# Performance work log

Measured on AMD Instinct MI355X. Metric: run time of the kernel, lower is better.

## Reference

```python
import jax, jax.numpy as jnp
import numpy as np
from jax import lax

B, S, H, SS, DS = 512, 200, 128, 2, 2  # batch, seq_len, hidden, static_size, dynamic_size

def _xavier(k, shape):
    fan_in, fan_out = shape[-1], shape[0]
    lim = float(np.sqrt(6.0 / (fan_in + fan_out)))
    return jax.random.uniform(k, shape, jnp.float32, -lim, lim)

def setup_inputs() -> dict:
    key = jax.random.key(0)
    ks = jax.random.split(key, 20)
    return {
        "static":  jax.random.uniform(ks[0], (B, SS, S), jnp.float32),
        "dynamic": jax.random.uniform(ks[1], (B, DS, S), jnp.float32),
        # Encoder: 1x1 Conv1d weights stored as [H, C] (kernel dim squeezed)
        "sW": _xavier(ks[2], (H, SS)),  "sb": jnp.zeros((H,), jnp.float32),
        "dW": _xavier(ks[3], (H, DS)),  "db": jnp.zeros((H,), jnp.float32),
        # Decoder learned initial output / hidden
        "x0": _xavier(ks[4], (1, SS)),  "h0": _xavier(ks[5], (1, H)),
        # Decoder input embedding Linear(SS -> H)
        "Wemb": _xavier(ks[6], (H, SS)), "bemb": jnp.zeros((H,), jnp.float32),
        # GRU (1 layer): torch layout [3H, H] gates ordered (r, z, n)
        "Wih": _xavier(ks[7], (3 * H, H)), "Whh": _xavier(ks[8], (3 * H, H)),
        "bih": jnp.zeros((3 * H,), jnp.float32), "bhh": jnp.zeros((3 * H,), jnp.float32),
        # Attention: v [H], W [H, 3H]
        "Wa": _xavier(ks[9], (H, 3 * H)), "va": _xavier(ks[10], (1, H))[0],
        # Decoder pointer head: v [H], W [H, 2H]
        "Wd": _xavier(ks[11], (H, 2 * H)), "vd": _xavier(ks[12], (1, H))[0],
    }

def _decode(static, dynamic, sW, sb, dW, db, x0, h0, Wemb, bemb,
            Wih, Whh, bih, bhh, Wa, va, Wd, vd):
    # Encoder: 1x1 convs == per-node linear maps  -> [B, H, S]
    static_enc  = jnp.einsum('hc,bcs->bhs', sW, static)  + sb[None, :, None]
    dynamic_enc = jnp.einsum('hc,bcs->bhs', dW, dynamic) + db[None, :, None]

    keys = jax.random.split(jax.random.key(42), S)  # one sample key per decode step
    static_sg = lax.stop_gradient(static)           # mirrors static.data gather in torch

    def step(carry, key):
        last_out, h = carry                              # [B,SS], [B,H]
        emb = last_out @ Wemb.T + bemb                   # [B,H]
        # GRU cell (torch gate order r, z, n)
        gi = emb @ Wih.T + bih                           # [B,3H]
        gh = h @ Whh.T + bhh
        r = jax.nn.sigmoid(gi[:, :H] + gh[:, :H])
        z = jax.nn.sigmoid(gi[:, H:2 * H] + gh[:, H:2 * H])
        n = jnp.tanh(gi[:, 2 * H:] + r * gh[:, 2 * H:])
        h_new = (1.0 - z) * n + z * h                    # [B,H]
        # Additive attention over nodes (vectorized over batch)
        hid = jnp.broadcast_to(h_new[:, :, None], (B, H, S))
        energy = jnp.concatenate([static_enc, dynamic_enc, hid], axis=1)   # [B,3H,S]
        attn = jax.nn.softmax(
            jnp.einsum('h,bhs->bs', va, jnp.tanh(jnp.einsum('hk,bks->bhs', Wa, energy))),
            axis=1)                                      # [B,S]
        context = jnp.einsum('bs,bhs->bh', attn, static_enc)               # [B,H]
        ctx = jnp.concatenate(
            [static_enc, jnp.broadcast_to(context[:, :, None], (B, H, S))], axis=1)  # [B,2H,S]
        logits = jnp.einsum('h,bhs->bs', vd,
                            jnp.tanh(jnp.einsum('hk,bks->bhs', Wd, ctx)))  # [B,S]
        # mask is all ones (mask_fn=None) -> log(mask)=0
        probs = jax.nn.softmax(logits, axis=1)
        idx = jax.random.categorical(key, logits, axis=1)                  # [B] int
        next_out = jnp.take_along_axis(static_sg, idx[:, None, None], axis=2)[:, :, 0]  # [B,SS]
        chosen_p = jnp.take_along_axis(probs, idx[:, None], axis=1)[:, 0]  # [B]
        return (next_out, h_new), (idx, chosen_p)

    init = (jnp.broadcast_to(x0, (B, SS)), jnp.broadcast_to(h0, (B, H)))
    _, (idx_seq, prob_seq) = lax.scan(step, init, keys)
    return idx_seq.T, prob_seq.T                          # [B,S] each

def reference(static, dynamic, sW, sb, dW, db, x0, h0, Wemb, bemb,
              Wih, Whh, bih, bhh, Wa, va, Wd, vd):
    return _decode(static, dynamic, sW, sb, dW, db, x0, h0, Wemb, bemb,
                   Wih, Whh, bih, bhh, Wa, va, Wd, vd)
```

## Files before the change

kernel.cpp:

```cpp
#include <hip/hip_runtime.h>
#include <stdint.h>
#include <math.h>

#define NB 512
#define NS 200
#define NH 128
#define NH3 384
#define NWAVE 8

#define IDX4(h) ((h) + (((h) >> 6) << 2))
#define IDX2(h) ((h) + (((h) >> 6) << 3))

__device__ __forceinline__ float xla_tanhf(float x) {
  float cx = fminf(fmaxf(x, -9.0f), 9.0f);
  float x2 = __fmul_rn(cx, cx);
  float p = -2.76076847742355e-16f;
  p = __fadd_rn(__fmul_rn(x2, p), 2.00018790482477e-13f);
  p = __fadd_rn(__fmul_rn(x2, p), -8.60467152213735e-11f);
  p = __fadd_rn(__fmul_rn(x2, p), 5.12229709037114e-08f);
  p = __fadd_rn(__fmul_rn(x2, p), 1.48572235717979e-05f);
  p = __fadd_rn(__fmul_rn(x2, p), 6.37261928875436e-04f);
  p = __fadd_rn(__fmul_rn(x2, p), 4.89352455891786e-03f);
  p = __fmul_rn(cx, p);
  float q = 1.19825839466702e-06f;
  q = __fadd_rn(__fmul_rn(x2, q), 1.18534705686654e-04f);
  q = __fadd_rn(__fmul_rn(x2, q), 2.26843463243900e-03f);
  q = __fadd_rn(__fmul_rn(x2, q), 4.89352518554385e-03f);
  float r = __fdiv_rn(p, q);
  return (fabsf(x) < 0.0004f) ? x : r;
}

__device__ __forceinline__ float xla_sigmoidf(float x) {
  return __fadd_rn(0.5f, __fmul_rn(0.5f, xla_tanhf(__fmul_rn(0.5f, x))));
}

__device__ __forceinline__ uint32_t rotl32(uint32_t v, int r) {
  return (v << r) | (v >> (32 - r));
}
__device__ __forceinline__ void threefry2x32(uint32_t k0, uint32_t k1,
                                             uint32_t x0, uint32_t x1,
                                             uint32_t& o0, uint32_t& o1) {
  uint32_t k2 = k0 ^ k1 ^ 0x1BD11BDAu;
  x0 += k0; x1 += k1;
  #define TFR(r) { x0 += x1; x1 = rotl32(x1, r); x1 ^= x0; }
  TFR(13) TFR(15) TFR(26) TFR(6)
  x0 += k1; x1 += k2 + 1u;
  TFR(17) TFR(29) TFR(16) TFR(24)
  x0 += k2; x1 += k0 + 2u;
  TFR(13) TFR(15) TFR(26) TFR(6)
  x0 += k0; x1 += k1 + 3u;
  TFR(17) TFR(29) TFR(16) TFR(24)
  x0 += k1; x1 += k2 + 4u;
  TFR(13) TFR(15) TFR(26) TFR(6)
  x0 += k2; x1 += k0 + 5u;
  #undef TFR
  o0 = x0; o1 = x1;
}

__device__ __forceinline__ float bits_to_gumbel(uint32_t bits) {
  const float kTiny = 1.1754943508222875e-38f;
  float f = __fsub_rn(__uint_as_float((bits >> 9) | 0x3F800000u), 1.0f);
  float u = __fadd_rn(__fmul_rn(f, __fsub_rn(1.0f, kTiny)), kTiny);
  u = fmaxf(kTiny, u);
  return -logf(-logf(u));
}

__global__ __launch_bounds__(512, 4) void k_decode(
    const float* __restrict__ stat, const float* __restrict__ dyn,
    const float* __restrict__ sW,   const float* __restrict__ sb,
    const float* __restrict__ dW,   const float* __restrict__ db,
    const float* __restrict__ x0,   const float* __restrict__ h0,
    const float* __restrict__ Wemb, const float* __restrict__ bemb,
    const float* __restrict__ Wih,  const float* __restrict__ Whh,
    const float* __restrict__ bih,  const float* __restrict__ bhh,
    const float* __restrict__ Wa,   const float* __restrict__ va,
    const float* __restrict__ Wd,   const float* __restrict__ vd,
    float* __restrict__ out) {

  __shared__ __align__(16) float st0L[NS], st1L[NS], dy0L[NS], dy1L[NS];
  __shared__ float4 AF4p[132];
  __shared__ float4 DF4p[132];
  __shared__ float4 CW4[NH];
  __shared__ float2 HtVaP[136];
  __shared__ float  AcL[NH];
  __shared__ float WembL[2*NH], bembL[NH];
  __shared__ float bihL[NH3], bhhL[NH3];
  __shared__ __align__(16) float embL[NH], hL[NH];
  __shared__ float giL[NH3], ghL[NH3];
  __shared__ float ex2L[NS], gumL[NS];
  __shared__ uint32_t keysL[2*NS];
  __shared__ float xpL[2];
  __shared__ float SvL[2];
  __shared__ float part[NWAVE][8];
  __shared__ int   partI[NWAVE];

  const int t = threadIdx.x;
  const int b = blockIdx.x;
  const int w = t >> 6;
  const int s = t >> 1;
  const int h0i = (t & 1) * 64;
  const int b4 = h0i + ((h0i >> 6) << 2);
  const int b2 = h0i + ((h0i >> 6) << 3);
  const bool activeS = (t < 2*NS);

  if (t < NS) {
    st0L[t] = stat[(size_t)b*2*NS + t];
    st1L[t] = stat[(size_t)b*2*NS + NS + t];
    dy0L[t] = dyn[(size_t)b*2*NS + t];
    dy1L[t] = dyn[(size_t)b*2*NS + NS + t];
    uint32_t q0, q1;
    threefry2x32(0u, 42u, 0u, (uint32_t)t, q0, q1);
    keysL[2*t] = q0; keysL[2*t + 1] = q1;
  }
  if (t < NH) {
    int h = t;
    const float* war = Wa + (size_t)h * NH3;
    float as0 = 0.f, as1 = 0.f, ad0 = 0.f, ad1 = 0.f, ac = 0.f;
    for (int k = 0; k < NH; ++k) {
      as0 = fmaf(war[k],     sW[k*2+0], as0);
      as1 = fmaf(war[k],     sW[k*2+1], as1);
      ad0 = fmaf(war[NH+k],  dW[k*2+0], ad0);
      ad1 = fmaf(war[NH+k],  dW[k*2+1], ad1);
      ac  = fmaf(war[k],     sb[k],     ac);
    }
    for (int k = 0; k < NH; ++k) ac = fmaf(war[NH+k], db[k], ac);
    AF4p[IDX4(h)] = make_float4(2.f*as0, 2.f*as1, 2.f*ad0, 2.f*ad1);
    HtVaP[IDX2(h)] = make_float2(va[h], 0.f);
    AcL[h] = ac;

    const float* wdr = Wd + (size_t)h * 256;
    float ds0 = 0.f, ds1 = 0.f, dc = 0.f, c0 = 0.f, c1 = 0.f, cb = 0.f;
    for (int k = 0; k < NH; ++k) {
      ds0 = fmaf(wdr[k],    sW[k*2+0], ds0);
      ds1 = fmaf(wdr[k],    sW[k*2+1], ds1);
      dc  = fmaf(wdr[k],    sb[k],     dc);
      c0  = fmaf(wdr[NH+k], sW[k*2+0], c0);
      c1  = fmaf(wdr[NH+k], sW[k*2+1], c1);
      cb  = fmaf(wdr[NH+k], sb[k],     cb);
    }
    DF4p[IDX4(h)] = make_float4(2.f*ds0, 2.f*ds1, vd[h], 0.f);
    CW4[h] = make_float4(2.f*c0, 2.f*c1, 2.f*cb, 2.f*dc);

    bembL[h] = bemb[h];
    WembL[2*h]   = Wemb[2*h];
    WembL[2*h+1] = Wemb[2*h+1];
    hL[h] = h0[h];
  }
  for (int i = t; i < NH3; i += 512) { bihL[i] = bih[i]; bhhL[i] = bhh[i]; }
  if (t == 0) {
    xpL[0] = x0[0]; xpL[1] = x0[1];
    float sva = 0.f, svd = 0.f;
    for (int h = 0; h < NH; ++h) { sva = __fadd_rn(sva, va[h]); svd = __fadd_rn(svd, vd[h]); }
    SvL[0] = sva; SvL[1] = svd;
  }
  __syncthreads();

  float s0r = 0.f, s1r = 0.f, d0r = 0.f, d1r = 0.f;
  if (activeS) { s0r = st0L[s]; s1r = st1L[s]; d0r = dy0L[s]; d1r = dy1L[s]; }
  const float svaR = SvL[0], svdR = SvL[1];

  for (int step = 0; step < NS; ++step) {
    if (t < NH) {
      float e = fmaf(xpL[1], WembL[t*2+1], __fmul_rn(xpL[0], WembL[t*2+0]));
      embL[t] = __fadd_rn(e, bembL[t]);
    } else if (t < NH + NS) {
      int si = t - NH;
      uint32_t k0 = keysL[2*step], k1 = keysL[2*step + 1];
      uint32_t q0, q1;
      threefry2x32(k0, k1, 0u, (uint32_t)(b*NS + si), q0, q1);
      gumL[si] = bits_to_gumbel(q0 ^ q1);
    }
    __syncthreads();

    if (t < 256) {
      const float4* wp0 = (const float4*)(Wih + (size_t)t * NH);
      const float4* wp1 = (const float4*)(Whh + (size_t)(NH + t) * NH);
      const float4* e4 = (const float4*)embL;
      const float4* h4 = (const float4*)hL;
      float a0 = 0.f, a1 = 0.f;
      #pragma unroll 8
      for (int k4 = 0; k4 < 32; ++k4) {
        float4 c0 = wp0[k4], c1 = wp1[k4];
        float4 ev = e4[k4],  hv = h4[k4];
        a0 = fmaf(c0.x, ev.x, a0); a0 = fmaf(c0.y, ev.y, a0);
        a0 = fmaf(c0.z, ev.z, a0); a0 = fmaf(c0.w, ev.w, a0);
        a1 = fmaf(c1.x, hv.x, a1); a1 = fmaf(c1.y, hv.y, a1);
        a1 = fmaf(c1.z, hv.z, a1); a1 = fmaf(c1.w, hv.w, a1);
      }
      giL[t]      = __fadd_rn(a0, bihL[t]);
      ghL[NH + t] = __fadd_rn(a1, bhhL[NH + t]);
    } else {
      const bool isWih = (t < NH3);
      const float4* wp = isWih
          ? (const float4*)(Wih + (size_t)t * NH)
          : (const float4*)(Whh + (size_t)(t - NH3) * NH);
      const float4* op = isWih ? (const float4*)embL : (const float4*)hL;
      float a0 = 0.f;
      #pragma unroll 8
      for (int k4 = 0; k4 < 32; ++k4) {
        float4 c = wp[k4], v = op[k4];
        a0 = fmaf(c.x, v.x, a0); a0 = fmaf(c.y, v.y, a0);
        a0 = fmaf(c.z, v.z, a0); a0 = fmaf(c.w, v.w, a0);
      }
      if (isWih) giL[t]       = __fadd_rn(a0, bihL[t]);
      else       ghL[t - NH3] = __fadd_rn(a0, bhhL[t - NH3]);
    }
    __syncthreads();

    if (t < NH) {
      float r = xla_sigmoidf(__fadd_rn(giL[t],      ghL[t]));
      float z = xla_sigmoidf(__fadd_rn(giL[t+NH],   ghL[t+NH]));
      float n = xla_tanhf(__fadd_rn(giL[t+2*NH], __fmul_rn(r, ghL[t+2*NH])));
      float hv = hL[t];
      hL[t] = __fadd_rn(__fmul_rn(__fsub_rn(1.0f, z), n), __fmul_rn(z, hv));
    }
    __syncthreads();

    if (t < NH) {
      const float4* war = (const float4*)(Wa + (size_t)t*NH3 + 2*NH);
      const float4* hn4 = (const float4*)hL;
      float acc = 0.f;
      #pragma unroll 8
      for (int k4 = 0; k4 < 32; ++k4) {
        float4 a = war[k4], hv = hn4[k4];
        acc = fmaf(a.x, hv.x, acc); acc = fmaf(a.y, hv.y, acc);
        acc = fmaf(a.z, hv.z, acc); acc = fmaf(a.w, hv.w, acc);
      }
      HtVaP[IDX2(t)].y = __fmul_rn(2.0f, __fadd_rn(acc, AcL[t]));
    }
    __syncthreads();

    float accE = 0.f;
    if (activeS) {
      #pragma unroll 4
      for (int j = 0; j < 64; ++j) {
        float4 af = AF4p[b4 + j];
        float2 hv = HtVaP[b2 + j];
        float e2 = fmaf(af.x, s0r, hv.y);
        e2 = fmaf(af.y, s1r, e2);
        e2 = fmaf(af.z, d0r, e2);
        e2 = fmaf(af.w, d1r, e2);
        float r = __builtin_amdgcn_rcpf(__fadd_rn(__expf(e2), 1.0f));
        accE = fmaf(hv.x, r, accE);
      }
    }
    float accSum = __fadd_rn(accE, __shfl_xor(accE, 1));
    float sc = activeS ? fmaf(-2.0f, accSum, svaR) : 0.f;

    float exv = activeS ? __expf(sc) : 0.f;
    {
      float sm = exv;
      float c0 = __fmul_rn(exv, s0r);
      float c1 = __fmul_rn(exv, s1r);
      #pragma unroll
      for (int mm = 2; mm < 64; mm <<= 1) {
        sm = __fadd_rn(sm, __shfl_xor(sm, mm));
        c0 = __fadd_rn(c0, __shfl_xor(c0, mm));
        c1 = __fadd_rn(c1, __shfl_xor(c1, mm));
      }
      if ((t & 63) == 0) { part[w][0] = sm; part[w][1] = c0; part[w][2] = c1; }
    }
    __syncthreads();

    if (t < NH) {
      float sume = part[0][0], r0 = part[0][1], r1 = part[0][2];
      #pragma unroll
      for (int ww = 1; ww < NWAVE; ++ww) {
        sume = __fadd_rn(sume, part[ww][0]);
        r0   = __fadd_rn(r0,   part[ww][1]);
        r1   = __fadd_rn(r1,   part[ww][2]);
      }
      r0 = __fdiv_rn(r0, sume); r1 = __fdiv_rn(r1, sume);
      float4 cw = CW4[t];
      float ct2 = fmaf(r0, cw.x, fmaf(r1, cw.y, cw.z));
      DF4p[IDX4(t)].w = __fadd_rn(cw.w, ct2);
    }
    __syncthreads();

    float accD = 0.f;
    if (activeS) {
      #pragma unroll 4
      for (int j = 0; j < 64; ++j) {
        float4 df = DF4p[b4 + j];
        float d2 = fmaf(df.x, s0r, df.w);
        d2 = fmaf(df.y, s1r, d2);
        float r = __builtin_amdgcn_rcpf(__fadd_rn(__expf(d2), 1.0f));
        accD = fmaf(df.z, r, accD);
      }
    }
    float accDS = __fadd_rn(accD, __shfl_xor(accD, 1));
    float sc2 = activeS ? fmaf(-2.0f, accDS, svdR) : 0.f;

    float e2 = activeS ? __expf(sc2) : 0.f;
    if (activeS && (t & 1) == 0) ex2L[s] = e2;
    {
      float gv = -INFINITY;
      int gidx = 1 << 20;
      if (activeS) {
        gv = __fadd_rn(gumL[s], sc2);
        gidx = s;
      }
      float sm = e2;
      #pragma unroll
      for (int mm = 2; mm < 64; mm <<= 1) {
        sm = __fadd_rn(sm, __shfl_xor(sm, mm));
        float ov = __shfl_xor(gv, mm); int oi = __shfl_xor(gidx, mm);
        if (ov > gv || (ov == gv && oi < gidx)) { gv = ov; gidx = oi; }
      }
      if ((t & 63) == 0) { part[w][3] = sm; part[w][4] = gv; partI[w] = gidx; }
    }
    __syncthreads();

    if (t == 0) {
      float bv = part[0][4]; int bi = partI[0];
      float sume2 = part[0][3];
      #pragma unroll
      for (int ww = 1; ww < NWAVE; ++ww) {
        float vv = part[ww][4]; int ii = partI[ww];
        if (vv > bv || (vv == bv && ii < bi)) { bv = vv; bi = ii; }
        sume2 = __fadd_rn(sume2, part[ww][3]);
      }
      out[(size_t)b*NS + step] = (float)bi;
      out[(size_t)NB*NS + (size_t)b*NS + step] = __fdiv_rn(ex2L[bi], sume2);
      xpL[0] = st0L[bi]; xpL[1] = st1L[bi];
    }
    __syncthreads();
  }
}

extern "C" void kernel_launch(void* const* d_in, const int* in_sizes, int n_in,
                              void* d_out, int out_size, void* d_ws, size_t ws_size,
                              hipStream_t stream) {
  (void)in_sizes; (void)n_in; (void)out_size; (void)d_ws; (void)ws_size;
  const float* stat = (const float*)d_in[0];
  const float* dyn  = (const float*)d_in[1];
  const float* sW   = (const float*)d_in[2];
  const float* sb   = (const float*)d_in[3];
  const float* dW   = (const float*)d_in[4];
  const float* db   = (const float*)d_in[5];
  const float* x0   = (const float*)d_in[6];
  const float* h0   = (const float*)d_in[7];
  const float* Wemb = (const float*)d_in[8];
  const float* bemb = (const float*)d_in[9];
  const float* Wih  = (const float*)d_in[10];
  const float* Whh  = (const float*)d_in[11];
  const float* bih  = (const float*)d_in[12];
  const float* bhh  = (const float*)d_in[13];
  const float* Wa   = (const float*)d_in[14];
  const float* va   = (const float*)d_in[15];
  const float* Wd   = (const float*)d_in[16];
  const float* vd   = (const float*)d_in[17];
  float* out = (float*)d_out;

  k_decode<<<NB, 512, 0, stream>>>(stat, dyn, sW, sb, dW, db, x0, h0,
                                   Wemb, bemb, Wih, Whh, bih, bhh,
                                   Wa, va, Wd, vd, out);
}
```

Before: 5.892 ms.

## Process two batch rows per block with 1024 threads sharing GRU weight loads

Each block now handles two batch elements (b and b+256) with 1024 threads. The GRU matvec loads each weight row once and applies it to both rows' embeddings and hidden states, which halves weight traffic per batch element. Per-row state is duplicated into A/B shared buffers, and the per-step reductions are split by half-block. The cost is half as many blocks (256 on the device), larger blocks with higher register and LDS pressure, and serial phases such as the attention matvec that still run on only 256 threads.

```diff
diff --git a/kernel.cpp b/kernel.cpp
--- a/kernel.cpp
+++ b/kernel.cpp
@@ -6,10 +6,11 @@
 #define NS 200
 #define NH 128
 #define NH3 384
-#define NWAVE 8
+#define NT 1024
+#define NWAVE 16
 
 #define IDX4(h) ((h) + (((h) >> 6) << 2))
-#define IDX2(h) ((h) + (((h) >> 6) << 3))
+#define IDX1(h) ((h) + (((h) >> 6) << 4))
 
 __device__ __forceinline__ float xla_tanhf(float x) {
   float cx = fminf(fmaxf(x, -9.0f), 9.0f);
@@ -65,7 +66,7 @@
   return -logf(-logf(u));
 }
 
-__global__ __launch_bounds__(512, 4) void k_decode(
+__global__ __launch_bounds__(NT, 4) void k_decode(
     const float* __restrict__ stat, const float* __restrict__ dyn,
     const float* __restrict__ sW,   const float* __restrict__ sb,
     const float* __restrict__ dW,   const float* __restrict__ db,
@@ -77,43 +78,55 @@
     const float* __restrict__ Wd,   const float* __restrict__ vd,
     float* __restrict__ out) {
 
-  __shared__ __align__(16) float st0L[NS], st1L[NS], dy0L[NS], dy1L[NS];
+  __shared__ __align__(16) float st0A[NS], st1A[NS], dy0A[NS], dy1A[NS];
+  __shared__ __align__(16) float st0B[NS], st1B[NS], dy0B[NS], dy1B[NS];
   __shared__ float4 AF4p[132];
-  __shared__ float4 DF4p[132];
+  __shared__ float4 DFSp[132];
   __shared__ float4 CW4[NH];
-  __shared__ float2 HtVaP[136];
+  __shared__ float  vaP[144];
+  __shared__ float  Ht2A[144], Ht2B[144];
+  __shared__ float  ct2A[144], ct2B[144];
   __shared__ float  AcL[NH];
   __shared__ float WembL[2*NH], bembL[NH];
   __shared__ float bihL[NH3], bhhL[NH3];
-  __shared__ __align__(16) float embL[NH], hL[NH];
-  __shared__ float giL[NH3], ghL[NH3];
-  __shared__ float ex2L[NS], gumL[NS];
+  __shared__ __align__(16) float embA[NH], embB[NH], hA[NH], hB[NH];
+  __shared__ float giA[NH3], ghA[NH3], giB[NH3], ghB[NH3];
+  __shared__ float ex2A[NS], ex2B[NS], gumA[NS], gumB[NS];
   __shared__ uint32_t keysL[2*NS];
-  __shared__ float xpL[2];
+  __shared__ float xpA[2], xpB[2];
   __shared__ float SvL[2];
   __shared__ float part[NWAVE][8];
   __shared__ int   partI[NWAVE];
 
   const int t = threadIdx.x;
-  const int b = blockIdx.x;
+  const int bA = blockIdx.x;
+  const int bB = blockIdx.x + 256;
   const int w = t >> 6;
-  const int s = t >> 1;
-  const int h0i = (t & 1) * 64;
+  const bool rB = (t >= 512);
+  const int tr = rB ? (t - 512) : t;
+  const int s = tr >> 1;
+  const int h0i = (tr & 1) * 64;
   const int b4 = h0i + ((h0i >> 6) << 2);
-  const int b2 = h0i + ((h0i >> 6) << 3);
-  const bool activeS = (t < 2*NS);
+  const int b1 = h0i + ((h0i >> 6) << 4);
+  const bool act = (tr < 2*NS);
 
   if (t < NS) {
-    st0L[t] = stat[(size_t)b*2*NS + t];
-    st1L[t] = stat[(size_t)b*2*NS + NS + t];
-    dy0L[t] = dyn[(size_t)b*2*NS + t];
-    dy1L[t] = dyn[(size_t)b*2*NS + NS + t];
+    st0A[t] = stat[(size_t)bA*2*NS + t];
+    st1A[t] = stat[(size_t)bA*2*NS + NS + t];
+    dy0A[t] = dyn[(size_t)bA*2*NS + t];
+    dy1A[t] = dyn[(size_t)bA*2*NS + NS + t];
     uint32_t q0, q1;
     threefry2x32(0u, 42u, 0u, (uint32_t)t, q0, q1);
     keysL[2*t] = q0; keysL[2*t + 1] = q1;
+  } else if (t >= 256 && t < 256 + NS) {
+    int si = t - 256;
+    st0B[si] = stat[(size_t)bB*2*NS + si];
+    st1B[si] = stat[(size_t)bB*2*NS + NS + si];
+    dy0B[si] = dyn[(size_t)bB*2*NS + si];
+    dy1B[si] = dyn[(size_t)bB*2*NS + NS + si];
   }
-  if (t < NH) {
-    int h = t;
+  if (t >= 512 && t < 512 + NH) {
+    int h = t - 512;
     const float* war = Wa + (size_t)h * NH3;
     float as0 = 0.f, as1 = 0.f, ad0 = 0.f, ad1 = 0.f, ac = 0.f;
     for (int k = 0; k < NH; ++k) {
@@ -125,7 +138,7 @@
     }
     for (int k = 0; k < NH; ++k) ac = fmaf(war[NH+k], db[k], ac);
     AF4p[IDX4(h)] = make_float4(2.f*as0, 2.f*as1, 2.f*ad0, 2.f*ad1);
-    HtVaP[IDX2(h)] = make_float2(va[h], 0.f);
+    vaP[IDX1(h)] = va[h];
     AcL[h] = ac;
 
     const float* wdr = Wd + (size_t)h * 256;
@@ -138,17 +151,19 @@
       c1  = fmaf(wdr[NH+k], sW[k*2+1], c1);
       cb  = fmaf(wdr[NH+k], sb[k],     cb);
     }
-    DF4p[IDX4(h)] = make_float4(2.f*ds0, 2.f*ds1, vd[h], 0.f);
+    DFSp[IDX4(h)] = make_float4(2.f*ds0, 2.f*ds1, vd[h], 0.f);
     CW4[h] = make_float4(2.f*c0, 2.f*c1, 2.f*cb, 2.f*dc);
 
     bembL[h] = bemb[h];
     WembL[2*h]   = Wemb[2*h];
     WembL[2*h+1] = Wemb[2*h+1];
-    hL[h] = h0[h];
+    hA[h] = h0[h];
+    hB[h] = h0[h];
   }
-  for (int i = t; i < NH3; i += 512) { bihL[i] = bih[i]; bhhL[i] = bhh[i]; }
+  for (int i = t; i < NH3; i += NT) { bihL[i] = bih[i]; bhhL[i] = bhh[i]; }
   if (t == 0) {
-    xpL[0] = x0[0]; xpL[1] = x0[1];
+    xpA[0] = x0[0]; xpA[1] = x0[1];
+    xpB[0] = x0[0]; xpB[1] = x0[1];
     float sva = 0.f, svd = 0.f;
     for (int h = 0; h < NH; ++h) { sva = __fadd_rn(sva, va[h]); svd = __fadd_rn(svd, vd[h]); }
     SvL[0] = sva; SvL[1] = svd;
@@ -156,69 +171,85 @@
   __syncthreads();
 
   float s0r = 0.f, s1r = 0.f, d0r = 0.f, d1r = 0.f;
-  if (activeS) { s0r = st0L[s]; s1r = st1L[s]; d0r = dy0L[s]; d1r = dy1L[s]; }
+  if (act) {
+    if (!rB) { s0r = st0A[s]; s1r = st1A[s]; d0r = dy0A[s]; d1r = dy1A[s]; }
+    else     { s0r = st0B[s]; s1r = st1B[s]; d0r = dy0B[s]; d1r = dy1B[s]; }
+  }
   const float svaR = SvL[0], svdR = SvL[1];
+  const float* HtX = rB ? Ht2B : Ht2A;
+  const float* ctX = rB ? ct2B : ct2A;
+  const float* gumX = rB ? gumB : gumA;
 
   for (int step = 0; step < NS; ++step) {
     if (t < NH) {
-      float e = fmaf(xpL[1], WembL[t*2+1], __fmul_rn(xpL[0], WembL[t*2+0]));
-      embL[t] = __fadd_rn(e, bembL[t]);
-    } else if (t < NH + NS) {
-      int si = t - NH;
+      float e = fmaf(xpA[1], WembL[t*2+1], __fmul_rn(xpA[0], WembL[t*2+0]));
+      embA[t] = __fadd_rn(e, bembL[t]);
+    } else if (t < 2*NH) {
+      int h = t - NH;
+      float e = fmaf(xpB[1], WembL[h*2+1], __fmul_rn(xpB[0], WembL[h*2+0]));
+      embB[h] = __fadd_rn(e, bembL[h]);
+    } else if (t < 2*NH + 2*NS) {
+      int gi = t - 2*NH;
       uint32_t k0 = keysL[2*step], k1 = keysL[2*step + 1];
       uint32_t q0, q1;
-      threefry2x32(k0, k1, 0u, (uint32_t)(b*NS + si), q0, q1);
-      gumL[si] = bits_to_gumbel(q0 ^ q1);
-    }
-    __syncthreads();
-
-    if (t < 256) {
-      const float4* wp0 = (const float4*)(Wih + (size_t)t * NH);
-      const float4* wp1 = (const float4*)(Whh + (size_t)(NH + t) * NH);
-      const float4* e4 = (const float4*)embL;
-      const float4* h4 = (const float4*)hL;
-      float a0 = 0.f, a1 = 0.f;
-      #pragma unroll 8
-      for (int k4 = 0; k4 < 32; ++k4) {
-        float4 c0 = wp0[k4], c1 = wp1[k4];
-        float4 ev = e4[k4],  hv = h4[k4];
-        a0 = fmaf(c0.x, ev.x, a0); a0 = fmaf(c0.y, ev.y, a0);
-        a0 = fmaf(c0.z, ev.z, a0); a0 = fmaf(c0.w, ev.w, a0);
-        a1 = fmaf(c1.x, hv.x, a1); a1 = fmaf(c1.y, hv.y, a1);
-        a1 = fmaf(c1.z, hv.z, a1); a1 = fmaf(c1.w, hv.w, a1);
-      }
-      giL[t]      = __fadd_rn(a0, bihL[t]);
-      ghL[NH + t] = __fadd_rn(a1, bhhL[NH + t]);
-    } else {
+      if (gi < NS) {
+        threefry2x32(k0, k1, 0u, (uint32_t)(bA*NS + gi), q0, q1);
+        gumA[gi] = bits_to_gumbel(q0 ^ q1);
+      } else {
+        int si = gi - NS;
+        threefry2x32(k0, k1, 0u, (uint32_t)(bB*NS + si), q0, q1);
+        gumB[si] = bits_to_gumbel(q0 ^ q1);
+      }
+    }
+    __syncthreads();
+
+    if (t < 2*NH3) {
       const bool isWih = (t < NH3);
       const float4* wp = isWih
           ? (const float4*)(Wih + (size_t)t * NH)
           : (const float4*)(Whh + (size_t)(t - NH3) * NH);
-      const float4* op = isWih ? (const float4*)embL : (const float4*)hL;
-      float a0 = 0.f;
+      const float4* opA = isWih ? (const float4*)embA : (const float4*)hA;
+      const float4* opB = isWih ? (const float4*)embB : (const float4*)hB;
+      float aA = 0.f, aB = 0.f;
       #pragma unroll 8
       for (int k4 = 0; k4 < 32; ++k4) {
-        float4 c = wp[k4], v = op[k4];
-        a0 = fmaf(c.x, v.x, a0); a0 = fmaf(c.y, v.y, a0);
-        a0 = fmaf(c.z, v.z, a0); a0 = fmaf(c.w, v.w, a0);
-      }
-      if (isWih) giL[t]       = __fadd_rn(a0, bihL[t]);
-      else       ghL[t - NH3] = __fadd_rn(a0, bhhL[t - NH3]);
+        float4 c = wp[k4];
+        float4 vA = opA[k4], vB = opB[k4];
+        aA = fmaf(c.x, vA.x, aA); aA = fmaf(c.y, vA.y, aA);
+        aA = fmaf(c.z, vA.z, aA); aA = fmaf(c.w, vA.w, aA);
+        aB = fmaf(c.x, vB.x, aB); aB = fmaf(c.y, vB.y, aB);
+        aB = fmaf(c.z, vB.z, aB); aB = fmaf(c.w, vB.w, aB);
+      }
+      if (isWih) {
+        giA[t] = __fadd_rn(aA, bihL[t]);
+        giB[t] = __fadd_rn(aB, bihL[t]);
+      } else {
+        int row = t - NH3;
+        ghA[row] = __fadd_rn(aA, bhhL[row]);
+        ghB[row] = __fadd_rn(aB, bhhL[row]);
+      }
     }
     __syncthreads();
 
     if (t < NH) {
-      float r = xla_sigmoidf(__fadd_rn(giL[t],      ghL[t]));
-      float z = xla_sigmoidf(__fadd_rn(giL[t+NH],   ghL[t+NH]));
-      float n = xla_tanhf(__fadd_rn(giL[t+2*NH], __fmul_rn(r, ghL[t+2*NH])));
-      float hv = hL[t];
-      hL[t] = __fadd_rn(__fmul_rn(__fsub_rn(1.0f, z), n), __fmul_rn(z, hv));
+      float r = xla_sigmoidf(__fadd_rn(giA[t],      ghA[t]));
+      float z = xla_sigmoidf(__fadd_rn(giA[t+NH],   ghA[t+NH]));
+      float n = xla_tanhf(__fadd_rn(giA[t+2*NH], __fmul_rn(r, ghA[t+2*NH])));
+      float hv = hA[t];
+      hA[t] = __fadd_rn(__fmul_rn(__fsub_rn(1.0f, z), n), __fmul_rn(z, hv));
+    } else if (t < 2*NH) {
+      int h = t - NH;
+      float r = xla_sigmoidf(__fadd_rn(giB[h],      ghB[h]));
+      float z = xla_sigmoidf(__fadd_rn(giB[h+NH],   ghB[h+NH]));
+      float n = xla_tanhf(__fadd_rn(giB[h+2*NH], __fmul_rn(r, ghB[h+2*NH])));
+      float hv = hB[h];
+      hB[h] = __fadd_rn(__fmul_rn(__fsub_rn(1.0f, z), n), __fmul_rn(z, hv));
     }
     __syncthreads();
 
     if (t < NH) {
       const float4* war = (const float4*)(Wa + (size_t)t*NH3 + 2*NH);
-      const float4* hn4 = (const float4*)hL;
+      const float4* hn4 = (const float4*)hA;
       float acc = 0.f;
       #pragma unroll 8
       for (int k4 = 0; k4 < 32; ++k4) {
@@ -226,28 +257,39 @@
         acc = fmaf(a.x, hv.x, acc); acc = fmaf(a.y, hv.y, acc);
         acc = fmaf(a.z, hv.z, acc); acc = fmaf(a.w, hv.w, acc);
       }
-      HtVaP[IDX2(t)].y = __fmul_rn(2.0f, __fadd_rn(acc, AcL[t]));
+      Ht2A[IDX1(t)] = __fmul_rn(2.0f, __fadd_rn(acc, AcL[t]));
+    } else if (t < 2*NH) {
+      int h = t - NH;
+      const float4* war = (const float4*)(Wa + (size_t)h*NH3 + 2*NH);
+      const float4* hn4 = (const float4*)hB;
+      float acc = 0.f;
+      #pragma unroll 8
+      for (int k4 = 0; k4 < 32; ++k4) {
+        float4 a = war[k4], hv = hn4[k4];
+        acc = fmaf(a.x, hv.x, acc); acc = fmaf(a.y, hv.y, acc);
+        acc = fmaf(a.z, hv.z, acc); acc = fmaf(a.w, hv.w, acc);
+      }
+      Ht2B[IDX1(h)] = __fmul_rn(2.0f, __fadd_rn(acc, AcL[h]));
     }
     __syncthreads();
 
     float accE = 0.f;
-    if (activeS) {
+    if (act) {
       #pragma unroll 4
       for (int j = 0; j < 64; ++j) {
         float4 af = AF4p[b4 + j];
-        float2 hv = HtVaP[b2 + j];
-        float e2 = fmaf(af.x, s0r, hv.y);
+        float e2 = fmaf(af.x, s0r, HtX[b1 + j]);
         e2 = fmaf(af.y, s1r, e2);
         e2 = fmaf(af.z, d0r, e2);
         e2 = fmaf(af.w, d1r, e2);
         float r = __builtin_amdgcn_rcpf(__fadd_rn(__expf(e2), 1.0f));
-        accE = fmaf(hv.x, r, accE);
+        accE = fmaf(vaP[b1 + j], r, accE);
       }
     }
     float accSum = __fadd_rn(accE, __shfl_xor(accE, 1));
-    float sc = activeS ? fmaf(-2.0f, accSum, svaR) : 0.f;
-
-    float exv = activeS ? __expf(sc) : 0.f;
+    float sc = act ? fmaf(-2.0f, accSum, svaR) : 0.f;
+
+    float exv = act ? __expf(sc) : 0.f;
     {
       float sm = exv;
       float c0 = __fmul_rn(exv, s0r);
@@ -262,45 +304,48 @@
     }
     __syncthreads();
 
-    if (t < NH) {
-      float sume = part[0][0], r0 = part[0][1], r1 = part[0][2];
+    if (t < 2*NH) {
+      int h = t & (NH - 1);
+      int base = (t < NH) ? 0 : 8;
+      float sume = part[base][0], r0 = part[base][1], r1 = part[base][2];
       #pragma unroll
-      for (int ww = 1; ww < NWAVE; ++ww) {
-        sume = __fadd_rn(sume, part[ww][0]);
-        r0   = __fadd_rn(r0,   part[ww][1]);
-        r1   = __fadd_rn(r1,   part[ww][2]);
+      for (int ww = 1; ww < 8; ++ww) {
+        sume = __fadd_rn(sume, part[base + ww][0]);
+        r0   = __fadd_rn(r0,   part[base + ww][1]);
+        r1   = __fadd_rn(r1,   part[base + ww][2]);
       }
       r0 = __fdiv_rn(r0, sume); r1 = __fdiv_rn(r1, sume);
-      float4 cw = CW4[t];
+      float4 cw = CW4[h];
       float ct2 = fmaf(r0, cw.x, fmaf(r1, cw.y, cw.z));
-      DF4p[IDX4(t)].w = __fadd_rn(cw.w, ct2);
+      if (t < NH) ct2A[IDX1(h)] = __fadd_rn(cw.w, ct2);
+      else        ct2B[IDX1(h)] = __fadd_rn(cw.w, ct2);
     }
     __syncthreads();
 
     float accD = 0.f;
-    if (activeS) {
+    if (act) {
       #pragma unroll 4
       for (int j = 0; j < 64; ++j) {
-        float4 df = DF4p[b4 + j];
-        float d2 = fmaf(df.x, s0r, df.w);
+        float4 df = DFSp[b4 + j];
+        float d2 = fmaf(df.x, s0r, ctX[b1 + j]);
         d2 = fmaf(df.y, s1r, d2);
         float r = __builtin_amdgcn_rcpf(__fadd_rn(__expf(d2), 1.0f));
         accD = fmaf(df.z, r, accD);
       }
     }
     float accDS = __fadd_rn(accD, __shfl_xor(accD, 1));
-    float sc2 = activeS ? fmaf(-2.0f, accDS, svdR) : 0.f;
-
-    float e2 = activeS ? __expf(sc2) : 0.f;
-    if (activeS && (t & 1) == 0) ex2L[s] = e2;
+    float sc2 = act ? fmaf(-2.0f, accDS, svdR) : 0.f;
+
+    float e2v = act ? __expf(sc2) : 0.f;
+    if (act && (tr & 1) == 0) { if (!rB) ex2A[s] = e2v; else ex2B[s] = e2v; }
     {
       float gv = -INFINITY;
       int gidx = 1 << 20;
-      if (activeS) {
-        gv = __fadd_rn(gumL[s], sc2);
+      if (act) {
+        gv = __fadd_rn(gumX[s], sc2);
         gidx = s;
       }
-      float sm = e2;
+      float sm = e2v;
       #pragma unroll
       for (int mm = 2; mm < 64; mm <<= 1) {
         sm = __fadd_rn(sm, __shfl_xor(sm, mm));
@@ -315,14 +360,26 @@
       float bv = part[0][4]; int bi = partI[0];
       float sume2 = part[0][3];
       #pragma unroll
-      for (int ww = 1; ww < NWAVE; ++ww) {
+      for (int ww = 1; ww < 8; ++ww) {
         float vv = part[ww][4]; int ii = partI[ww];
         if (vv > bv || (vv == bv && ii < bi)) { bv = vv; bi = ii; }
         sume2 = __fadd_rn(sume2, part[ww][3]);
       }
-      out[(size_t)b*NS + step] = (float)bi;
-      out[(size_t)NB*NS + (size_t)b*NS + step] = __fdiv_rn(ex2L[bi], sume2);
-      xpL[0] = st0L[bi]; xpL[1] = st1L[bi];
+      out[(size_t)bA*NS + step] = (float)bi;
+      out[(size_t)NB*NS + (size_t)bA*NS + step] = __fdiv_rn(ex2A[bi], sume2);
+      xpA[0] = st0A[bi]; xpA[1] = st1A[bi];
+    } else if (t == 512) {
+      float bv = part[8][4]; int bi = partI[8];
+      float sume2 = part[8][3];
+      #pragma unroll
+      for (int ww = 9; ww < 16; ++ww) {
+        float vv = part[ww][4]; int ii = partI[ww];
+        if (vv > bv || (vv == bv && ii < bi)) { bv = vv; bi = ii; }
+        sume2 = __fadd_rn(sume2, part[ww][3]);
+      }
+      out[(size_t)bB*NS + step] = (float)bi;
+      out[(size_t)NB*NS + (size_t)bB*NS + step] = __fdiv_rn(ex2B[bi], sume2);
+      xpB[0] = st0B[bi]; xpB[1] = st1B[bi];
     }
     __syncthreads();
   }
@@ -352,7 +409,7 @@
   const float* vd   = (const float*)d_in[17];
   float* out = (float*)d_out;
 
-  k_decode<<<NB, 512, 0, stream>>>(stat, dyn, sW, sb, dW, db, x0, h0,
-                                   Wemb, bemb, Wih, Whh, bih, bhh,
-                                   Wa, va, Wd, vd, out);
-}
+  k_decode<<<NB/2, NT, 0, stream>>>(stat, dyn, sW, sb, dW, db, x0, h0,
+                                    Wemb, bemb, Wih, Whh, bih, bhh,
+                                    Wa, va, Wd, vd, out);
+}
```

New measurement: 5.487 ms. 1.07x faster.
